# Kernel tuning notes

Measured on AMD Instinct MI355X. Metric: run time of the kernel, lower is better.

Reference implementation:

```python
import jax, jax.numpy as jnp
import numpy as np
import math


def _sinusoidal_pe(seq_len, hidden_dim, dtype):
    pos = jnp.arange(seq_len, dtype=jnp.float32)[:, None]              # [S,1]
    div = jnp.exp(jnp.arange(0, hidden_dim, 2, dtype=jnp.float32) * (-math.log(10000.0) / hidden_dim))  # [H/2]
    ang = pos * div                                                    # [S,H/2]
    pe = jnp.stack([jnp.sin(ang), jnp.cos(ang)], axis=-1).reshape(seq_len, hidden_dim)  # interleave sin/cos
    return pe.astype(dtype)


def setup_inputs() -> dict:
    key = jax.random.key(0)
    ks = jax.random.split(key, 12)
    B, S, H = 4, 2048, 1024
    scale = 1.0 / math.sqrt(H)
    inp = {
        "x": jax.random.normal(ks[0], (B, S, H), dtype=jnp.float32),
        "mask": jax.random.randint(ks[1], (B, S, S), 0, 2, dtype=jnp.int32),
        "Wq": jax.random.normal(ks[2], (H, H), dtype=jnp.float32) * scale,
        "bq": jax.random.normal(ks[3], (H,), dtype=jnp.float32) * 0.02,
        "Wk": jax.random.normal(ks[4], (H, H), dtype=jnp.float32) * scale,
        "bk": jax.random.normal(ks[5], (H,), dtype=jnp.float32) * 0.02,
        "Wv": jax.random.normal(ks[6], (H, H), dtype=jnp.float32) * scale,
        "bv": jax.random.normal(ks[7], (H,), dtype=jnp.float32) * 0.02,
        "pos_bias": jax.random.normal(ks[8], (S, S), dtype=jnp.float32),
        "Wo": jax.random.normal(ks[9], (H, H), dtype=jnp.float32) * scale,
        "bo": jax.random.normal(ks[10], (H,), dtype=jnp.float32) * 0.02,
        "gamma": jnp.ones((H,), dtype=jnp.float32),
        "beta": jnp.zeros((H,), dtype=jnp.float32),
    }
    return inp


def reference(x, mask, Wq, bq, Wk, bk, Wv, bv, pos_bias, Wo, bo, gamma, beta):
    B, S, H = x.shape
    scale = math.sqrt(H)
    pe = _sinusoidal_pe(S, H, x.dtype)                  # [S,H]
    xp = x + pe[None, :, :]                             # [B,S,H]
    # torch Linear: y = x @ W.T + b
    q = jnp.einsum('bsh,oh->bso', xp, Wq) + bq
    k = jnp.einsum('bsh,oh->bso', xp, Wk) + bk
    v = jnp.einsum('bsh,oh->bso', xp, Wv) + bv
    scores = jnp.einsum('bqh,bkh->bqk', q, k) / scale   # [B,S,S]
    scores = scores + pos_bias[None, :S, :S]
    scores = jnp.where(mask == 0, jnp.asarray(-1e9, scores.dtype), scores)
    attn = jax.nn.softmax(scores, axis=-1)              # dropout = identity (eval mode)
    context = jnp.einsum('bqk,bkh->bqh', attn, v)
    out = jnp.einsum('bsh,oh->bso', context, Wo) + bo
    # LayerNorm(out + x)
    h = out + x
    mu = jnp.mean(h, axis=-1, keepdims=True)
    var = jnp.var(h, axis=-1, keepdims=True)
    normed = (h - mu) * jax.lax.rsqrt(var + 1e-5) * gamma + beta
    return normed, attn
```

## Files before the change

kernel.cpp:

```cpp
#include <hip/hip_runtime.h>
#include <hip/hip_bf16.h>
#include <math.h>

typedef __hip_bfloat16 bf16;
typedef __bf16 bf16x8 __attribute__((ext_vector_type(8)));
typedef float f32x4 __attribute__((ext_vector_type(4)));

static constexpr int  B_  = 4, S_ = 2048, H_ = 1024;
static constexpr long BSH = (long)B_ * S_ * H_;
static constexpr long SH  = (long)S_ * H_;
static constexpr long SS  = (long)S_ * S_;
static constexpr long HH  = (long)H_ * H_;

#define GLOAD_LDS16(gp, lp)                                                          \
  __builtin_amdgcn_global_load_lds((__attribute__((address_space(1))) void*)(gp),    \
                                   (__attribute__((address_space(3))) void*)(lp),    \
                                   16, 0, 0)

#define BARRIER() do { __builtin_amdgcn_s_barrier(); asm volatile("" ::: "memory"); } while (0)

template <int N> __device__ __forceinline__ void waitcnt_vm() {
  if constexpr (N == 0)      asm volatile("s_waitcnt vmcnt(0)" ::: "memory");
  else if constexpr (N == 8) asm volatile("s_waitcnt vmcnt(8)" ::: "memory");
}

__device__ __forceinline__ float wave_reduce_sum(float v) {
#pragma unroll
  for (int o = 32; o; o >>= 1) v += __shfl_xor(v, o, 64);
  return v;
}
__device__ __forceinline__ float bf16r(float v) {
  return __bfloat162float(__float2bfloat16(v));
}

__global__ void prep_kernel(const float* __restrict__ Wq, const float* __restrict__ Wk,
                            const float* __restrict__ Wv, const float* __restrict__ Wo,
                            bf16* __restrict__ wdst,
                            const float* __restrict__ x, bf16* __restrict__ xpb,
                            const int* __restrict__ mask, unsigned* __restrict__ mask_bits,
                            const float* __restrict__ pos_bias, bf16* __restrict__ pbb) {
  const int bx  = blockIdx.x;
  const int tid = threadIdx.x;
  if (bx < 4096) {
    const int w = bx >> 10;
    const float* src = (w == 0) ? Wq : (w == 1) ? Wk : (w == 2) ? Wv : Wo;
    bf16* d = wdst + (long)w * HH;
    const int idx = ((bx & 1023) << 8) + tid;
    const float4 f = ((const float4*)src)[idx];
    d[idx * 4 + 0] = __float2bfloat16(f.x);
    d[idx * 4 + 1] = __float2bfloat16(f.y);
    d[idx * 4 + 2] = __float2bfloat16(f.z);
    d[idx * 4 + 3] = __float2bfloat16(f.w);
  } else if (bx < 20480) {
    const long idx = (((long)(bx - 4096)) << 8) + tid;
    const int  i   = (int)(idx & (H_ / 2 - 1));
    const long bs  = idx >> 9;
    const int  s   = (int)(bs & (S_ - 1));
    const float div = __expf((float)(2 * i) * (-9.210340371976184f / (float)H_));
    const float ang = (float)s * div;
    const float2 xv = ((const float2*)x)[idx];
    xpb[idx * 2 + 0] = __float2bfloat16(xv.x + __sinf(ang));
    xpb[idx * 2 + 1] = __float2bfloat16(xv.y + __cosf(ang));
  } else if (bx < 22528) {
    const long uidx = (((long)(bx - 20480)) << 8) + tid;
    const int4* mp  = (const int4*)mask + uidx * 8;
    unsigned bits = 0;
#pragma unroll
    for (int q = 0; q < 8; ++q) {
      const int4 v = mp[q];
      bits |= (v.x ? 1u : 0u) << (q * 4 + 0);
      bits |= (v.y ? 1u : 0u) << (q * 4 + 1);
      bits |= (v.z ? 1u : 0u) << (q * 4 + 2);
      bits |= (v.w ? 1u : 0u) << (q * 4 + 3);
    }
    mask_bits[uidx] = bits;
  } else {
    const long idx = (((long)(bx - 22528)) << 8) + tid;
    const float4 f = ((const float4*)pos_bias)[idx];
    bf16* d = pbb + idx * 4;
    d[0] = __float2bfloat16(f.x);
    d[1] = __float2bfloat16(f.y);
    d[2] = __float2bfloat16(f.z);
    d[3] = __float2bfloat16(f.w);
  }
}

template <int MODE, bool DBUF>
__global__ void gemm_nt(const bf16* __restrict__ A, long sA,
                        const bf16* __restrict__ Bm, long sB,
                        bf16* __restrict__ Cb, float* __restrict__ Cf, long sC,
                        int M, int N, int K,
                        const float* __restrict__ bias0,
                        const float* __restrict__ bias1,
                        const float* __restrict__ bias2,
                        const bf16* __restrict__ pos_bias,
                        const unsigned* __restrict__ mask_bits,
                        const float* __restrict__ xres,
                        const float* __restrict__ inv_sum) {
  constexpr int BM = 128, BN = 128, BK = 64;
  constexpr int NBUF = DBUF ? 2 : 1;
  __shared__ bf16 As[NBUF][BM * BK];
  __shared__ bf16 Bs[NBUF][BN * BK];

  const int tid  = threadIdx.x;
  const int lane = tid & 63;
  const int wave = tid >> 6;
  const int wm   = wave & 1;
  const int wn   = wave >> 1;
  const int z    = blockIdx.z;
  const int m0   = blockIdx.x * BM;
  const int n0   = blockIdx.y * BN;

  const bf16* Ab = A  + (long)z * sA;
  const bf16* Bb = Bm + (long)z * sB;

  const int rw = tid >> 3;
  const int cp = (tid & 7) ^ (rw & 7);
  const bf16* ga = Ab + (long)(m0 + rw) * K + cp * 8;
  const bf16* gb = Bb + (long)(n0 + rw) * K + cp * 8;

  auto stage = [&](int tile, int buf) {
    const long k0 = (long)tile * BK;
#pragma unroll
    for (int q = 0; q < 4; ++q) {
      GLOAD_LDS16(ga + (long)(32 * q) * K + k0, &As[buf][tid * 8 + q * 2048]);
      GLOAD_LDS16(gb + (long)(32 * q) * K + k0, &Bs[buf][tid * 8 + q * 2048]);
    }
  };

  f32x4 acc[4][4] = {};

  const int fr     = lane & 15;
  const int k0slot = lane >> 4;
  const int sw     = fr & 7;

  auto tile_compute = [&](const char* bAc, const char* bBc) {
#pragma unroll
    for (int ks = 0; ks < 2; ++ks) {
      const int co = ((k0slot + 4 * ks) ^ sw) << 4;
      bf16x8 af[4], bfv[4];
#pragma unroll
      for (int i = 0; i < 4; ++i) {
        af[i]  = *(const bf16x8*)(bAc + (wm * 64 + i * 16 + fr) * 128 + co);
        bfv[i] = *(const bf16x8*)(bBc + (wn * 64 + i * 16 + fr) * 128 + co);
      }
#pragma unroll
      for (int i = 0; i < 4; ++i)
#pragma unroll
        for (int j = 0; j < 4; ++j)
          acc[i][j] = __builtin_amdgcn_mfma_f32_16x16x32_bf16(af[i], bfv[j], acc[i][j], 0, 0, 0);
    }
  };

  const int nkt = K / BK;
  if constexpr (DBUF) {
    stage(0, 0);
    for (int kt = 0; kt < nkt; ++kt) {
      const int cur = kt & 1;
      if (kt + 1 < nkt) {
        stage(kt + 1, (cur ^ 1) & (NBUF - 1));
        waitcnt_vm<8>();
      } else {
        waitcnt_vm<0>();
      }
      BARRIER();
      tile_compute((const char*)&As[cur][0], (const char*)&Bs[cur][0]);
      BARRIER();
    }
  } else {
    for (int kt = 0; kt < nkt; ++kt) {
      stage(kt, 0);
      __syncthreads();
      tile_compute((const char*)&As[0][0], (const char*)&Bs[0][0]);
      __syncthreads();
    }
  }

  const float* biasz = (MODE == 0) ? ((z == 0) ? bias0 : bias1) : bias0;

  const int cc = lane & 15;
  const int cr = (lane >> 4) * 4;
#pragma unroll
  for (int i = 0; i < 4; ++i) {
    const int rowb = m0 + wm * 64 + i * 16 + cr;
#pragma unroll
    for (int j = 0; j < 4; ++j) {
      const int col = n0 + wn * 64 + j * 16 + cc;
#pragma unroll
      for (int r = 0; r < 4; ++r) {
        const int  row  = rowb + r;
        const long loff = (long)row * N + col;
        const long off  = (long)z * sC + loff;
        const float v   = acc[i][j][r];
        if (MODE == 0) {
          float o = v + biasz[col];
          if (z == 0) o *= 0.03125f;
          Cb[off] = __float2bfloat16(o);
        } else if (MODE == 1) {
          const unsigned mw = mask_bits[off >> 5];
          float sc = v + __bfloat162float(pos_bias[loff]);
          if (((mw >> (col & 31)) & 1u) == 0u) sc = -1e9f;
          Cb[off] = __float2bfloat16(__expf(fminf(sc, 60.0f)));
        } else if (MODE == 2) {
          Cb[off] = __float2bfloat16(v * inv_sum[z * S_ + row]);
        } else if (MODE == 3) {
          Cf[off] = v + biasz[col] + xres[off];
        } else {
          Cb[off] = __float2bfloat16(v + bias0[row]);
        }
      }
    }
  }
}

__global__ void rownorm_kernel(const bf16* __restrict__ E, float* __restrict__ attn_f,
                               float* __restrict__ inv_sum) {
  const long row = blockIdx.x;
  const int  tid = threadIdx.x;
  const uint4 d = *(const uint4*)(E + row * (long)S_ + tid * 8);
  float ev[8];
  ev[0] = __uint_as_float(d.x << 16); ev[1] = __uint_as_float(d.x & 0xffff0000u);
  ev[2] = __uint_as_float(d.y << 16); ev[3] = __uint_as_float(d.y & 0xffff0000u);
  ev[4] = __uint_as_float(d.z << 16); ev[5] = __uint_as_float(d.z & 0xffff0000u);
  ev[6] = __uint_as_float(d.w << 16); ev[7] = __uint_as_float(d.w & 0xffff0000u);
  float s = 0.f;
#pragma unroll
  for (int i = 0; i < 8; ++i) s += ev[i];
  s = wave_reduce_sum(s);
  __shared__ float red[4];
  if ((tid & 63) == 0) red[tid >> 6] = s;
  __syncthreads();
  const float inv = 1.0f / fmaxf(red[0] + red[1] + red[2] + red[3], 1e-30f);
  if (tid == 0) inv_sum[row] = inv;
  float4 o0, o1;
  o0.x = bf16r(ev[0] * inv); o0.y = bf16r(ev[1] * inv);
  o0.z = bf16r(ev[2] * inv); o0.w = bf16r(ev[3] * inv);
  o1.x = bf16r(ev[4] * inv); o1.y = bf16r(ev[5] * inv);
  o1.z = bf16r(ev[6] * inv); o1.w = bf16r(ev[7] * inv);
  float4* dst = (float4*)(attn_f + row * (long)S_ + tid * 8);
  dst[0] = o0;
  dst[1] = o1;
}

__global__ void ln_kernel(float* __restrict__ h, const float* __restrict__ gamma,
                          const float* __restrict__ beta) {
  const long row = blockIdx.x;
  float* hr = h + row * (long)H_;
  const int tid = threadIdx.x;
  const float4 v4 = ((const float4*)hr)[tid];
  float s = v4.x + v4.y + v4.z + v4.w;
  s = wave_reduce_sum(s);
  __shared__ float redA[4], redB[4];
  if ((tid & 63) == 0) redA[tid >> 6] = s;
  __syncthreads();
  const float mu = (redA[0] + redA[1] + redA[2] + redA[3]) * (1.0f / H_);
  const float dx = v4.x - mu, dy = v4.y - mu, dz = v4.z - mu, dw = v4.w - mu;
  float vs = dx * dx + dy * dy + dz * dz + dw * dw;
  vs = wave_reduce_sum(vs);
  if ((tid & 63) == 0) redB[tid >> 6] = vs;
  __syncthreads();
  const float var  = (redB[0] + redB[1] + redB[2] + redB[3]) * (1.0f / H_);
  const float rstd = rsqrtf(var + 1e-5f);
  const float4 g4 = ((const float4*)gamma)[tid];
  const float4 b4 = ((const float4*)beta)[tid];
  float4 o;
  o.x = bf16r(dx * rstd * g4.x + b4.x);
  o.y = bf16r(dy * rstd * g4.y + b4.y);
  o.z = bf16r(dz * rstd * g4.z + b4.z);
  o.w = bf16r(dw * rstd * g4.w + b4.w);
  ((float4*)hr)[tid] = o;
}

extern "C" void kernel_launch(void* const* d_in, const int* in_sizes, int n_in,
                              void* d_out, int out_size, void* d_ws, size_t ws_size,
                              hipStream_t stream) {
  const float* x        = (const float*)d_in[0];
  const int*   mask     = (const int*)d_in[1];
  const float* Wq       = (const float*)d_in[2];
  const float* bq       = (const float*)d_in[3];
  const float* Wk       = (const float*)d_in[4];
  const float* bk       = (const float*)d_in[5];
  const float* Wv       = (const float*)d_in[6];
  const float* bv       = (const float*)d_in[7];
  const float* pos_bias = (const float*)d_in[8];
  const float* Wo       = (const float*)d_in[9];
  const float* bo       = (const float*)d_in[10];
  const float* gamma    = (const float*)d_in[11];
  const float* beta     = (const float*)d_in[12];

  float* normed_f = (float*)d_out;
  float* attn_f   = (float*)((char*)d_out + ((size_t)32 << 20));

  const size_t MiB = (size_t)1 << 20;
  bf16*     xpb       = (bf16*)d_ws;
  bf16*     q_b       = (bf16*)((char*)d_ws +  16 * MiB);
  bf16*     kbuf      = (bf16*)((char*)d_ws +  32 * MiB);
  bf16*     vT        = (bf16*)((char*)d_ws +  64 * MiB);
  bf16*     ctx       = (bf16*)((char*)d_ws +  80 * MiB);
  bf16*     attn_b    = (bf16*)((char*)d_ws +  96 * MiB);
  bf16*     wts       = (bf16*)((char*)d_ws + 128 * MiB);
  float*    inv_sum   = (float*)((char*)d_ws + 136 * MiB);
  unsigned* mask_bits = (unsigned*)((char*)d_ws + 137 * MiB);
  bf16*     pbb       = (bf16*)((char*)d_ws + 139 * MiB);
  bf16* Wqb = wts, *Wvb = wts + 2 * HH, *Wob = wts + 3 * HH;

  const int MQKV = B_ * S_;

  prep_kernel<<<dim3(26624), 256, 0, stream>>>(Wq, Wk, Wv, Wo, wts, x, xpb,
                                               mask, mask_bits, pos_bias, pbb);

  gemm_nt<0, false><<<dim3(64, 8, 2), 256, 0, stream>>>(xpb, 0, Wqb, HH, q_b, nullptr, BSH,
                                                        MQKV, H_, H_, bq, bk, nullptr,
                                                        nullptr, nullptr, nullptr, nullptr);

  gemm_nt<4, false><<<dim3(8, 16, 4), 256, 0, stream>>>(Wvb, 0, xpb, SH, vT, nullptr, SH,
                                                        H_, S_, H_, bv, nullptr, nullptr,
                                                        nullptr, nullptr, nullptr, nullptr);

  gemm_nt<1, false><<<dim3(16, 16, B_), 256, 0, stream>>>(q_b, SH, kbuf, SH,
                                                          attn_b, nullptr, SS,
                                                          S_, S_, H_, nullptr, nullptr, nullptr,
                                                          pbb, mask_bits, nullptr, nullptr);

  rownorm_kernel<<<B_ * S_, 256, 0, stream>>>(attn_b, attn_f, inv_sum);

  gemm_nt<2, true><<<dim3(16, 8, B_), 256, 0, stream>>>(attn_b, SS, vT, SH,
                                                        ctx, nullptr, SH,
                                                        S_, H_, S_, nullptr, nullptr, nullptr,
                                                        nullptr, nullptr, nullptr, inv_sum);

  gemm_nt<3, false><<<dim3(64, 8, 1), 256, 0, stream>>>(ctx, 0, Wob, 0, nullptr, normed_f, 0,
                                                        MQKV, H_, H_, bo, nullptr, nullptr,
                                                        nullptr, nullptr, x, nullptr);

  ln_kernel<<<B_ * S_, 256, 0, stream>>>(normed_f, gamma, beta);
}
```

Measured before the change: 424.1 us.

## Fuse all stages into a persistent cooperative mega-kernel with grid syncs

Replaces the seven separate launches with one cooperative persistent kernel of 1024 blocks that loops over virtual block indices per stage and uses grid-wide syncs between stages. The Q/K and V projection GEMMs now share one stage. The aim is to cut launch gaps and tail effects between kernels. In exchange, the attn@V GEMM loses its double-buffered LDS pipeline, since the mega-kernel uses single-buffer shared memory. Occupancy is capped by launch bounds and the cooperative grid size, and the old launch path is kept as a fallback if the cooperative launch fails.

```diff
diff --git a/kernel.cpp b/kernel.cpp
--- a/kernel.cpp
+++ b/kernel.cpp
@@ -1,6 +1,9 @@
 #include <hip/hip_runtime.h>
+#include <hip/hip_cooperative_groups.h>
 #include <hip/hip_bf16.h>
 #include <math.h>
+
+namespace cg = cooperative_groups;
 
 typedef __hip_bfloat16 bf16;
 typedef __bf16 bf16x8 __attribute__((ext_vector_type(8)));
@@ -33,13 +36,11 @@
   return __bfloat162float(__float2bfloat16(v));
 }
 
-__global__ void prep_kernel(const float* __restrict__ Wq, const float* __restrict__ Wk,
-                            const float* __restrict__ Wv, const float* __restrict__ Wo,
-                            bf16* __restrict__ wdst,
-                            const float* __restrict__ x, bf16* __restrict__ xpb,
-                            const int* __restrict__ mask, unsigned* __restrict__ mask_bits,
-                            const float* __restrict__ pos_bias, bf16* __restrict__ pbb) {
-  const int bx  = blockIdx.x;
+
+__device__ __forceinline__ void prep_core(
+    int bx, const float* Wq, const float* Wk, const float* Wv, const float* Wo,
+    bf16* wdst, const float* x, bf16* xpb,
+    const int* mask, unsigned* mask_bits, const float* pos_bias, bf16* pbb) {
   const int tid = threadIdx.x;
   if (bx < 4096) {
     const int w = bx >> 10;
@@ -86,30 +87,23 @@
 }
 
 template <int MODE, bool DBUF>
-__global__ void gemm_nt(const bf16* __restrict__ A, long sA,
-                        const bf16* __restrict__ Bm, long sB,
-                        bf16* __restrict__ Cb, float* __restrict__ Cf, long sC,
-                        int M, int N, int K,
-                        const float* __restrict__ bias0,
-                        const float* __restrict__ bias1,
-                        const float* __restrict__ bias2,
-                        const bf16* __restrict__ pos_bias,
-                        const unsigned* __restrict__ mask_bits,
-                        const float* __restrict__ xres,
-                        const float* __restrict__ inv_sum) {
+__device__ __forceinline__ void gemm_core(
+    bf16* As, bf16* Bs, int bxx, int byy, int z,
+    const bf16* A, long sA, const bf16* Bm, long sB,
+    bf16* Cb, float* Cf, long sC, int M, int N, int K,
+    const float* bias0, const float* bias1,
+    const bf16* pbb, const unsigned* mask_bits,
+    const float* xres, const float* inv_sum) {
   constexpr int BM = 128, BN = 128, BK = 64;
-  constexpr int NBUF = DBUF ? 2 : 1;
-  __shared__ bf16 As[NBUF][BM * BK];
-  __shared__ bf16 Bs[NBUF][BN * BK];
+  constexpr int TILE = BM * BK;
 
   const int tid  = threadIdx.x;
   const int lane = tid & 63;
   const int wave = tid >> 6;
   const int wm   = wave & 1;
   const int wn   = wave >> 1;
-  const int z    = blockIdx.z;
-  const int m0   = blockIdx.x * BM;
-  const int n0   = blockIdx.y * BN;
+  const int m0   = bxx * BM;
+  const int n0   = byy * BN;
 
   const bf16* Ab = A  + (long)z * sA;
   const bf16* Bb = Bm + (long)z * sB;
@@ -123,8 +117,8 @@
     const long k0 = (long)tile * BK;
 #pragma unroll
     for (int q = 0; q < 4; ++q) {
-      GLOAD_LDS16(ga + (long)(32 * q) * K + k0, &As[buf][tid * 8 + q * 2048]);
-      GLOAD_LDS16(gb + (long)(32 * q) * K + k0, &Bs[buf][tid * 8 + q * 2048]);
+      GLOAD_LDS16(ga + (long)(32 * q) * K + k0, As + buf * TILE + tid * 8 + q * 2048);
+      GLOAD_LDS16(gb + (long)(32 * q) * K + k0, Bs + buf * TILE + tid * 8 + q * 2048);
     }
   };
 
@@ -158,26 +152,25 @@
     for (int kt = 0; kt < nkt; ++kt) {
       const int cur = kt & 1;
       if (kt + 1 < nkt) {
-        stage(kt + 1, (cur ^ 1) & (NBUF - 1));
+        stage(kt + 1, cur ^ 1);
         waitcnt_vm<8>();
       } else {
         waitcnt_vm<0>();
       }
       BARRIER();
-      tile_compute((const char*)&As[cur][0], (const char*)&Bs[cur][0]);
+      tile_compute((const char*)(As + cur * TILE), (const char*)(Bs + cur * TILE));
       BARRIER();
     }
   } else {
     for (int kt = 0; kt < nkt; ++kt) {
       stage(kt, 0);
       __syncthreads();
-      tile_compute((const char*)&As[0][0], (const char*)&Bs[0][0]);
+      tile_compute((const char*)As, (const char*)Bs);
       __syncthreads();
     }
   }
 
   const float* biasz = (MODE == 0) ? ((z == 0) ? bias0 : bias1) : bias0;
-
   const int cc = lane & 15;
   const int cr = (lane >> 4) * 4;
 #pragma unroll
@@ -198,7 +191,7 @@
           Cb[off] = __float2bfloat16(o);
         } else if (MODE == 1) {
           const unsigned mw = mask_bits[off >> 5];
-          float sc = v + __bfloat162float(pos_bias[loff]);
+          float sc = v + __bfloat162float(pbb[loff]);
           if (((mw >> (col & 31)) & 1u) == 0u) sc = -1e9f;
           Cb[off] = __float2bfloat16(__expf(fminf(sc, 60.0f)));
         } else if (MODE == 2) {
@@ -213,10 +206,9 @@
   }
 }
 
-__global__ void rownorm_kernel(const bf16* __restrict__ E, float* __restrict__ attn_f,
-                               float* __restrict__ inv_sum) {
-  const long row = blockIdx.x;
-  const int  tid = threadIdx.x;
+__device__ __forceinline__ void rownorm_core(float* red, long row, const bf16* E,
+                                             float* attn_f, float* inv_sum) {
+  const int tid = threadIdx.x;
   const uint4 d = *(const uint4*)(E + row * (long)S_ + tid * 8);
   float ev[8];
   ev[0] = __uint_as_float(d.x << 16); ev[1] = __uint_as_float(d.x & 0xffff0000u);
@@ -227,10 +219,10 @@
 #pragma unroll
   for (int i = 0; i < 8; ++i) s += ev[i];
   s = wave_reduce_sum(s);
-  __shared__ float red[4];
   if ((tid & 63) == 0) red[tid >> 6] = s;
   __syncthreads();
   const float inv = 1.0f / fmaxf(red[0] + red[1] + red[2] + red[3], 1e-30f);
+  __syncthreads();
   if (tid == 0) inv_sum[row] = inv;
   float4 o0, o1;
   o0.x = bf16r(ev[0] * inv); o0.y = bf16r(ev[1] * inv);
@@ -242,15 +234,14 @@
   dst[1] = o1;
 }
 
-__global__ void ln_kernel(float* __restrict__ h, const float* __restrict__ gamma,
-                          const float* __restrict__ beta) {
-  const long row = blockIdx.x;
+__device__ __forceinline__ void ln_core(float* redA, float* redB, long row,
+                                        float* h, const float* gamma,
+                                        const float* beta) {
   float* hr = h + row * (long)H_;
   const int tid = threadIdx.x;
   const float4 v4 = ((const float4*)hr)[tid];
   float s = v4.x + v4.y + v4.z + v4.w;
   s = wave_reduce_sum(s);
-  __shared__ float redA[4], redB[4];
   if ((tid & 63) == 0) redA[tid >> 6] = s;
   __syncthreads();
   const float mu = (redA[0] + redA[1] + redA[2] + redA[3]) * (1.0f / H_);
@@ -271,6 +262,115 @@
   ((float4*)hr)[tid] = o;
 }
 
+struct KArgs {
+  const float* x; const int* mask;
+  const float* Wq; const float* bq; const float* Wk; const float* bk;
+  const float* Wv; const float* bv; const float* pos_bias;
+  const float* Wo; const float* bo; const float* gamma; const float* beta;
+  float* normed_f; float* attn_f;
+  bf16* xpb; bf16* q_b; bf16* kbuf; bf16* vT; bf16* ctx; bf16* attn_b;
+  bf16* wts; float* inv_sum; unsigned* mask_bits; bf16* pbb;
+};
+
+__global__ void __launch_bounds__(256, 4) mega_kernel(KArgs a) {
+  __shared__ bf16  As[128 * 64];
+  __shared__ bf16  Bs[128 * 64];
+  __shared__ float sred[8];
+  cg::grid_group grid = cg::this_grid();
+  const int nb = gridDim.x;
+
+  for (int vb = blockIdx.x; vb < 26624; vb += nb)
+    prep_core(vb, a.Wq, a.Wk, a.Wv, a.Wo, a.wts, a.x, a.xpb,
+              a.mask, a.mask_bits, a.pos_bias, a.pbb);
+  grid.sync();
+
+  for (int vb = blockIdx.x; vb < 1536; vb += nb) {
+    if (vb < 1024) {
+      const int bx = vb & 63, by = (vb >> 6) & 7, z = vb >> 9;
+      gemm_core<0, false>(As, Bs, bx, by, z, a.xpb, 0, a.wts, HH,
+                          a.q_b, nullptr, BSH, B_ * S_, H_, H_,
+                          a.bq, a.bk, nullptr, nullptr, nullptr, nullptr);
+    } else {
+      const int w = vb - 1024, bx = w & 7, by = (w >> 3) & 15, z = w >> 7;
+      gemm_core<4, false>(As, Bs, bx, by, z, a.wts + 2 * HH, 0, a.xpb, SH,
+                          a.vT, nullptr, SH, H_, S_, H_,
+                          a.bv, nullptr, nullptr, nullptr, nullptr, nullptr);
+    }
+  }
+  grid.sync();
+
+  for (int vb = blockIdx.x; vb < 1024; vb += nb) {
+    const int bx = vb & 15, by = (vb >> 4) & 15, z = vb >> 8;
+    gemm_core<1, false>(As, Bs, bx, by, z, a.q_b, SH, a.kbuf, SH,
+                        a.attn_b, nullptr, SS, S_, S_, H_,
+                        nullptr, nullptr, a.pbb, a.mask_bits, nullptr, nullptr);
+  }
+  grid.sync();
+
+  for (int vb = blockIdx.x; vb < B_ * S_; vb += nb)
+    rownorm_core(sred, vb, a.attn_b, a.attn_f, a.inv_sum);
+  grid.sync();
+
+  for (int vb = blockIdx.x; vb < 512; vb += nb) {
+    const int bx = vb & 15, by = (vb >> 4) & 7, z = vb >> 7;
+    gemm_core<2, false>(As, Bs, bx, by, z, a.attn_b, SS, a.vT, SH,
+                        a.ctx, nullptr, SH, S_, H_, S_,
+                        nullptr, nullptr, nullptr, nullptr, nullptr, a.inv_sum);
+  }
+  grid.sync();
+
+  for (int vb = blockIdx.x; vb < 512; vb += nb) {
+    const int bx = vb & 63, by = vb >> 6;
+    gemm_core<3, false>(As, Bs, bx, by, 0, a.ctx, 0, a.wts + 3 * HH, 0,
+                        nullptr, a.normed_f, 0, B_ * S_, H_, H_,
+                        a.bo, nullptr, nullptr, nullptr, a.x, nullptr);
+  }
+  grid.sync();
+
+  for (int vb = blockIdx.x; vb < B_ * S_; vb += nb)
+    ln_core(sred, sred + 4, vb, a.normed_f, a.gamma, a.beta);
+}
+
+__global__ void prep_kernel(const float* __restrict__ Wq, const float* __restrict__ Wk,
+                            const float* __restrict__ Wv, const float* __restrict__ Wo,
+                            bf16* __restrict__ wdst,
+                            const float* __restrict__ x, bf16* __restrict__ xpb,
+                            const int* __restrict__ mask, unsigned* __restrict__ mask_bits,
+                            const float* __restrict__ pos_bias, bf16* __restrict__ pbb) {
+  prep_core(blockIdx.x, Wq, Wk, Wv, Wo, wdst, x, xpb, mask, mask_bits, pos_bias, pbb);
+}
+
+template <int MODE, bool DBUF>
+__global__ void gemm_nt(const bf16* __restrict__ A, long sA,
+                        const bf16* __restrict__ Bm, long sB,
+                        bf16* __restrict__ Cb, float* __restrict__ Cf, long sC,
+                        int M, int N, int K,
+                        const float* __restrict__ bias0,
+                        const float* __restrict__ bias1,
+                        const bf16* __restrict__ pbb,
+                        const unsigned* __restrict__ mask_bits,
+                        const float* __restrict__ xres,
+                        const float* __restrict__ inv_sum) {
+  constexpr int NBUF = DBUF ? 2 : 1;
+  __shared__ bf16 As[NBUF * 128 * 64];
+  __shared__ bf16 Bs[NBUF * 128 * 64];
+  gemm_core<MODE, DBUF>(As, Bs, blockIdx.x, blockIdx.y, blockIdx.z,
+                        A, sA, Bm, sB, Cb, Cf, sC, M, N, K,
+                        bias0, bias1, pbb, mask_bits, xres, inv_sum);
+}
+
+__global__ void rownorm_kernel(const bf16* __restrict__ E, float* __restrict__ attn_f,
+                               float* __restrict__ inv_sum) {
+  __shared__ float red[4];
+  rownorm_core(red, blockIdx.x, E, attn_f, inv_sum);
+}
+
+__global__ void ln_kernel(float* __restrict__ h, const float* __restrict__ gamma,
+                          const float* __restrict__ beta) {
+  __shared__ float redA[4], redB[4];
+  ln_core(redA, redB, blockIdx.x, h, gamma, beta);
+}
+
 extern "C" void kernel_launch(void* const* d_in, const int* in_sizes, int n_in,
                               void* d_out, int out_size, void* d_ws, size_t ws_size,
                               hipStream_t stream) {
@@ -302,36 +402,41 @@
   float*    inv_sum   = (float*)((char*)d_ws + 136 * MiB);
   unsigned* mask_bits = (unsigned*)((char*)d_ws + 137 * MiB);
   bf16*     pbb       = (bf16*)((char*)d_ws + 139 * MiB);
-  bf16* Wqb = wts, *Wvb = wts + 2 * HH, *Wob = wts + 3 * HH;
+  bf16* Wvb = wts + 2 * HH, *Wob = wts + 3 * HH;
 
   const int MQKV = B_ * S_;
+
+  KArgs ha;
+  ha.x = x; ha.mask = mask; ha.Wq = Wq; ha.bq = bq; ha.Wk = Wk; ha.bk = bk;
+  ha.Wv = Wv; ha.bv = bv; ha.pos_bias = pos_bias; ha.Wo = Wo; ha.bo = bo;
+  ha.gamma = gamma; ha.beta = beta; ha.normed_f = normed_f; ha.attn_f = attn_f;
+  ha.xpb = xpb; ha.q_b = q_b; ha.kbuf = kbuf; ha.vT = vT; ha.ctx = ctx;
+  ha.attn_b = attn_b; ha.wts = wts; ha.inv_sum = inv_sum;
+  ha.mask_bits = mask_bits; ha.pbb = pbb;
+  void* kp[] = { &ha };
+  hipError_t err = hipLaunchCooperativeKernel((void*)mega_kernel, dim3(1024),
+                                              dim3(256), kp, 0, stream);
+  if (err == hipSuccess) return;
 
   prep_kernel<<<dim3(26624), 256, 0, stream>>>(Wq, Wk, Wv, Wo, wts, x, xpb,
                                                mask, mask_bits, pos_bias, pbb);
-
-  gemm_nt<0, false><<<dim3(64, 8, 2), 256, 0, stream>>>(xpb, 0, Wqb, HH, q_b, nullptr, BSH,
-                                                        MQKV, H_, H_, bq, bk, nullptr,
+  gemm_nt<0, false><<<dim3(64, 8, 2), 256, 0, stream>>>(xpb, 0, wts, HH, q_b, nullptr, BSH,
+                                                        MQKV, H_, H_, bq, bk,
                                                         nullptr, nullptr, nullptr, nullptr);
-
   gemm_nt<4, false><<<dim3(8, 16, 4), 256, 0, stream>>>(Wvb, 0, xpb, SH, vT, nullptr, SH,
-                                                        H_, S_, H_, bv, nullptr, nullptr,
+                                                        H_, S_, H_, bv, nullptr,
                                                         nullptr, nullptr, nullptr, nullptr);
-
   gemm_nt<1, false><<<dim3(16, 16, B_), 256, 0, stream>>>(q_b, SH, kbuf, SH,
                                                           attn_b, nullptr, SS,
-                                                          S_, S_, H_, nullptr, nullptr, nullptr,
+                                                          S_, S_, H_, nullptr, nullptr,
                                                           pbb, mask_bits, nullptr, nullptr);
-
   rownorm_kernel<<<B_ * S_, 256, 0, stream>>>(attn_b, attn_f, inv_sum);
-
   gemm_nt<2, true><<<dim3(16, 8, B_), 256, 0, stream>>>(attn_b, SS, vT, SH,
                                                         ctx, nullptr, SH,
-                                                        S_, H_, S_, nullptr, nullptr, nullptr,
+                                                        S_, H_, S_, nullptr, nullptr,
                                                         nullptr, nullptr, nullptr, inv_sum);
-
   gemm_nt<3, false><<<dim3(64, 8, 1), 256, 0, stream>>>(ctx, 0, Wob, 0, nullptr, normed_f, 0,
-                                                        MQKV, H_, H_, bo, nullptr, nullptr,
+                                                        MQKV, H_, H_, bo, nullptr,
                                                         nullptr, nullptr, x, nullptr);
-
   ln_kernel<<<B_ * S_, 256, 0, stream>>>(normed_f, gamma, beta);
 }
```

Measured after the change: 1.208 ms. 185% more time.
